# Performance work log

Hardware: AMD Instinct MI355X
Metric: run time of the kernel (lower is better)

Reference implementation:

```python
import jax, jax.numpy as jnp
import numpy as np

N_FFT = 2048
STRIDE = 512
FREQ_BINS = N_FFT  # __init__ passes freq_bins=n_fft


def _fourier_kernels():
    s = np.arange(N_FFT, dtype=np.float64)
    # scipy get_window('hann', n_fft, fftbins=True)
    win = 0.5 - 0.5 * np.cos(2.0 * np.pi * s / N_FFT)
    k = np.arange(FREQ_BINS, dtype=np.float64)
    phase = 2.0 * np.pi * np.outer(k, s) / N_FFT  # (bins, n_fft)
    wsin = (win * np.sin(phase)).astype(np.float32)
    wcos = (win * np.cos(phase)).astype(np.float32)
    return wsin, wcos


def setup_inputs() -> dict:
    key = jax.random.key(0)
    x = jax.random.normal(key, (8, 262144), dtype=jnp.float32)
    wsin, wcos = _fourier_kernels()
    return {"x": x, "wsin": jnp.asarray(wsin), "wcos": jnp.asarray(wcos)}


def reference(x, wsin, wcos):
    # center=True, pad_mode='reflect'
    xp = jnp.pad(x, ((0, 0), (N_FFT // 2, N_FFT // 2)), mode="reflect")
    num_frames = (xp.shape[1] - N_FFT) // STRIDE + 1
    # frame the signal: (batch, num_frames, n_fft)
    idx = np.arange(num_frames)[:, None] * STRIDE + np.arange(N_FFT)
    frames = xp[:, idx]
    # dense DFT as GEMM (equivalent to conv1d with sin/cos filters)
    imag = jnp.einsum("btn,kn->bkt", frames, wsin)
    real = jnp.einsum("btn,kn->bkt", frames, wcos)
    return (real, -imag)
```

## Files before the change

### kernel.cpp

```cpp
#include <hip/hip_runtime.h>
#include <hip/hip_bf16.h>
#include <stdint.h>

#define XLEN   262144
#define NT     513
#define NTP    528
#define NB     8
#define NCOL   (NB * NTP)
#define NKC4   320
#define KQ     512
#define NK     1088
#define NFFT   2048
#define OUTKT  (2048 * NT)
#define WSTR   ((size_t)NKC4 * KQ)
#define FSTR   ((size_t)NCOL * KQ)
#define PSTR   ((size_t)NKC4 * NCOL)

typedef __attribute__((ext_vector_type(8))) short short8;
typedef __attribute__((ext_vector_type(4))) short short4v;
typedef __attribute__((ext_vector_type(2))) short short2v;
typedef __attribute__((ext_vector_type(4))) float f32x4;

__device__ __forceinline__ short cvt_bf16(float f) {
  return __builtin_bit_cast(short, (__bf16)f);
}

__device__ __forceinline__ f32x4 bf4_to_f32(short4v v) {
  f32x4 o;
#pragma unroll
  for (int e = 0; e < 4; ++e) {
    uint32_t u = ((uint32_t)(uint16_t)v[e]) << 16;
    o[e] = __builtin_bit_cast(float, u);
  }
  return o;
}

__device__ __forceinline__ void gload16(const short* g, const short* l) {
  __builtin_amdgcn_global_load_lds(
      (const __attribute__((address_space(1))) void*)g,
      (__attribute__((address_space(3))) void*)l, 16, 0, 0);
}


__global__ __launch_bounds__(256) void conv_w_split4(
    const float* __restrict__ wsin, const float* __restrict__ wcos,
    short* __restrict__ wc4, short* __restrict__ ws4) {
  const int row = blockIdx.x;
  const int n0 = threadIdx.x * 8;
  const int m0 = n0 >> 2;
  short2v c[4], s[4];
  if (row <= 256) {
    const float* pc = wcos + (size_t)row * NFFT + n0;
    const float* ps = wsin + (size_t)row * NFFT + n0;
    f32x4 c0 = *(const f32x4*)pc, c1 = *(const f32x4*)(pc + 4);
    f32x4 s0 = *(const f32x4*)ps, s1 = *(const f32x4*)(ps + 4);
#pragma unroll
    for (int r = 0; r < 4; ++r) {
      c[r][0] = cvt_bf16(c0[r]); c[r][1] = cvt_bf16(c1[r]);
      s[r][0] = cvt_bf16(s0[r]); s[r][1] = cvt_bf16(s1[r]);
    }
  } else {
#pragma unroll
    for (int r = 0; r < 4; ++r) { c[r][0] = 0; c[r][1] = 0; s[r][0] = 0; s[r][1] = 0; }
  }
#pragma unroll
  for (int r = 0; r < 4; ++r) {
    *(short2v*)&wc4[r * WSTR + (size_t)row * KQ + m0] = c[r];
    *(short2v*)&ws4[r * WSTR + (size_t)row * KQ + m0] = s[r];
  }
}

__global__ __launch_bounds__(256) void conv_fr_split4(const float* __restrict__ x,
                                                      short* __restrict__ fr4) {
  const int j = blockIdx.x;
  const int b = j / NTP;
  const int t = j - b * NTP;
  const int n0 = threadIdx.x * 8;
  const int m0 = n0 >> 2;
  short2v v[4];
  if (t < NT) {
    const float* xb = x + (size_t)b * XLEN;
    const int q0 = t * 512 + n0 - 1024;
    float f[8];
    if (q0 >= 0 && q0 + 7 < XLEN) {
      *(f32x4*)(f)     = *(const f32x4*)(xb + q0);
      *(f32x4*)(f + 4) = *(const f32x4*)(xb + q0 + 4);
    } else {
#pragma unroll
      for (int e = 0; e < 8; ++e) {
        int mm = q0 + e;
        mm = (mm < 0) ? -mm : mm;
        mm = (mm >= XLEN) ? (2 * XLEN - 2 - mm) : mm;
        f[e] = xb[mm];
      }
    }
#pragma unroll
    for (int r = 0; r < 4; ++r) { v[r][0] = cvt_bf16(f[r]); v[r][1] = cvt_bf16(f[4 + r]); }
  } else {
#pragma unroll
    for (int r = 0; r < 4; ++r) { v[r][0] = 0; v[r][1] = 0; }
  }
#pragma unroll
  for (int r = 0; r < 4; ++r)
    *(short2v*)&fr4[r * FSTR + (size_t)j * KQ + m0] = v[r];
}

__global__ __launch_bounds__(256, 3) void dft_gemm_split4(
    const short* __restrict__ wc4, const short* __restrict__ ws4,
    const short* __restrict__ fr4,
    short* __restrict__ pC4, short* __restrict__ pS4) {
  __shared__ short lds[16384];

  const int tid  = threadIdx.x;
  const int lane = tid & 63;
  const int wid  = tid >> 6;

  const int o   = blockIdx.x;
  const int xcd = o & 7;
  const int i   = o >> 3;
  const int wg  = ((xcd < 4) ? xcd * 83 : 332 + (xcd - 4) * 82) + i;
  const int side = wg / 165;
  const int w    = wg - side * 165;
  const int k0   = (w % 5) * 64;
  const int j0   = (w / 5) * 128;

  const short* Ac = wc4 + side * WSTR;
  const short* As = ws4 + side * WSTR;
  const short* Bf = fr4 + side * FSTR;
  short* pC = pC4 + side * PSTR;
  short* pS = pS4 + side * PSTR;

  const int wrow = (wid >> 1) * 32;
  const int wcol = (wid & 1) * 64;

  f32x4 accC[2][4], accS[2][4];
#pragma unroll
  for (int m = 0; m < 2; ++m)
#pragma unroll
    for (int n = 0; n < 4; ++n) { accC[m][n] = (f32x4)0.0f; accS[m][n] = (f32x4)0.0f; }

  const int fr_r = lane & 15;
  const int srow = lane >> 3;
  const int scol = ((lane & 7) ^ srow) * 8;

  auto stage = [&](int n0) {
#pragma unroll
    for (int i2 = 0; i2 < 8; ++i2) {
      const int q = wid * 8 + i2;
      const short* src;
      int dst;
      if (q < 8) {
        src = Ac + (size_t)(k0 + q * 8 + srow) * KQ + n0 + scol;
        dst = q * 512;
      } else if (q < 16) {
        src = As + (size_t)(k0 + (q - 8) * 8 + srow) * KQ + n0 + scol;
        dst = 4096 + (q - 8) * 512;
      } else {
        src = Bf + (size_t)(j0 + (q - 16) * 8 + srow) * KQ + n0 + scol;
        dst = 8192 + (q - 16) * 512;
      }
      gload16(src, &lds[dst]);
    }
  };

  for (int ts = 0; ts < 8; ++ts) {
    if (ts) __syncthreads();
    stage(ts * 64);
    __syncthreads();
#pragma unroll
    for (int ks = 0; ks < 2; ++ks) {
      const int cc = ks * 4 + (lane >> 4);
      short8 aC[2], aS[2], bF[4];
#pragma unroll
      for (int m = 0; m < 2; ++m) {
        const int r = wrow + m * 16 + fr_r;
        const int off = (r << 6) + ((cc ^ (r & 7)) << 3);
        aC[m] = *(const short8*)&lds[off];
        aS[m] = *(const short8*)&lds[4096 + off];
      }
#pragma unroll
      for (int n = 0; n < 4; ++n) {
        const int r = wcol + n * 16 + fr_r;
        const int off = (r << 6) + ((cc ^ (r & 7)) << 3);
        bF[n] = *(const short8*)&lds[8192 + off];
      }
#pragma unroll
      for (int m = 0; m < 2; ++m)
#pragma unroll
        for (int n = 0; n < 4; ++n) {
          accC[m][n] = __builtin_amdgcn_mfma_f32_16x16x32_bf16(aC[m], bF[n], accC[m][n], 0, 0, 0);
          accS[m][n] = __builtin_amdgcn_mfma_f32_16x16x32_bf16(aS[m], bF[n], accS[m][n], 0, 0, 0);
        }
    }
  }

#pragma unroll
  for (int m = 0; m < 2; ++m) {
    const int row = k0 + wrow + m * 16 + (lane >> 4) * 4;
#pragma unroll
    for (int n = 0; n < 4; ++n) {
      const int col = j0 + wcol + n * 16 + (lane & 15);
      const size_t base = (size_t)row * NCOL + col;
#pragma unroll
      for (int r = 0; r < 4; ++r) {
        pC[base + (size_t)r * NCOL] = cvt_bf16(accC[m][n][r]);
        pS[base + (size_t)r * NCOL] = cvt_bf16(accS[m][n][r]);
      }
    }
  }
}

__global__ __launch_bounds__(256) void combine4_kernel(
    const short* __restrict__ pC4, const short* __restrict__ pS4,
    float* __restrict__ outR, float* __restrict__ outI) {
  const int k  = blockIdx.y;
  const int jq = blockIdx.x * 256 + threadIdx.x;
  if (jq >= NCOL / 4) return;
  const int j = jq * 4;
  const int b = j / NTP;
  const int t = j - b * NTP;
  const size_t pb = (size_t)k * NCOL + j;
  f32x4 C[4], S[4];
#pragma unroll
  for (int r = 0; r < 4; ++r) {
    C[r] = bf4_to_f32(*(const short4v*)&pC4[r * PSTR + pb]);
    S[r] = bf4_to_f32(*(const short4v*)&pS4[r * PSTR + pb]);
  }
  const f32x4 CA = C[0] + C[2], CB = C[1] + C[3];
  const f32x4 CmA = C[0] - C[2], CmB = C[1] - C[3];
  const f32x4 SA = S[0] + S[2], SB = S[1] + S[3];
  const f32x4 SmA = S[0] - S[2], SmB = S[1] - S[3];

  f32x4 Cw[4], Sw[4];
  Cw[0] = CA + CB;   Sw[0] = SA + SB;
  Cw[1] = CmA - SmB; Sw[1] = SmA + CmB;
  Cw[2] = CA - CB;   Sw[2] = SA - SB;
  Cw[3] = CmA + SmB; Sw[3] = SmA - CmB;

  const size_t ob = (size_t)b * OUTKT + t;
  const bool mir = (k >= 1) && (k <= 255);
#pragma unroll
  for (int jj = 0; jj < 4; ++jj) {
    const int rowD = 512 * jj + k;
    float* rD = outR + ob + (size_t)rowD * NT;
    float* iD = outI + ob + (size_t)rowD * NT;
    const int rowM = 512 * (4 - jj) - k;
    float* rM = outR + ob + (size_t)rowM * NT;
    float* iM = outI + ob + (size_t)rowM * NT;
#pragma unroll
    for (int e = 0; e < 4; ++e) {
      if (t + e < NT) {
        rD[e] = Cw[jj][e];
        iD[e] = -Sw[jj][e];
        if (mir) { rM[e] = Cw[jj][e]; iM[e] = Sw[jj][e]; }
      }
    }
  }
}


__global__ __launch_bounds__(256) void conv_w_kernel(const float* __restrict__ wsin,
                                                     const float* __restrict__ wcos,
                                                     short* __restrict__ wc,
                                                     short* __restrict__ ws) {
  const int row = blockIdx.x;
  const int c = threadIdx.x * 8;
  const float* src = (blockIdx.y ? wsin : wcos) + (size_t)row * NFFT + c;
  short* dst = (blockIdx.y ? ws : wc) + (size_t)row * NFFT + c;
  f32x4 a = *(const f32x4*)src;
  f32x4 b = *(const f32x4*)(src + 4);
  short8 o;
#pragma unroll
  for (int j = 0; j < 4; ++j) { o[j] = cvt_bf16(a[j]); o[4 + j] = cvt_bf16(b[j]); }
  *(short8*)dst = o;
}

__global__ __launch_bounds__(256) void conv_frames_kernel(const float* __restrict__ x,
                                                          short* __restrict__ fr) {
  const int j = blockIdx.x;
  const int b = j / NTP;
  const int t = j - b * NTP;
  const int c = threadIdx.x * 8;
  short8 o;
  if (t >= NT) {
#pragma unroll
    for (int k = 0; k < 8; ++k) o[k] = 0;
  } else {
    const float* xb = x + (size_t)b * XLEN;
    const int base = t * 512 + c - 1024;
    float v[8];
    if (base >= 0 && base + 7 < XLEN) {
      *(f32x4*)(v)     = *(const f32x4*)(xb + base);
      *(f32x4*)(v + 4) = *(const f32x4*)(xb + base + 4);
    } else {
#pragma unroll
      for (int k = 0; k < 8; ++k) {
        int m = base + k;
        m = (m < 0) ? -m : m;
        m = (m >= XLEN) ? (2 * XLEN - 2 - m) : m;
        v[k] = xb[m];
      }
    }
#pragma unroll
    for (int k = 0; k < 8; ++k) o[k] = cvt_bf16(v[k]);
  }
  *(short8*)&fr[(size_t)j * NFFT + c] = o;
}

__global__ __launch_bounds__(256, 3) void dft_gemm_r4(
    const short* __restrict__ wc_bf,
    const short* __restrict__ ws_bf,
    const short* __restrict__ fr_bf,
    float* __restrict__ outR,
    float* __restrict__ outI) {
  __shared__ short lds[16384];

  const int tid  = threadIdx.x;
  const int lane = tid & 63;
  const int wid  = tid >> 6;

  const int o   = blockIdx.x;
  const int xcd = o & 7;
  const int wg  = ((xcd < 1) ? xcd * 71 : 71 + (xcd - 1) * 70) + (o >> 3);
  const int k0  = (wg % 17) * 64;
  const int j0  = (wg / 17) * 128;

  const int wrow = (wid >> 1) * 32;
  const int wcol = (wid & 1) * 64;

  f32x4 accR[2][4], accI[2][4];
#pragma unroll
  for (int m = 0; m < 2; ++m)
#pragma unroll
    for (int n = 0; n < 4; ++n) { accR[m][n] = (f32x4)0.0f; accI[m][n] = (f32x4)0.0f; }

  const int fr_r = lane & 15;
  const int srow = lane >> 3;
  const int scol = ((lane & 7) ^ srow) * 8;

  auto stage = [&](int n0) {
#pragma unroll
    for (int i = 0; i < 8; ++i) {
      const int q = wid * 8 + i;
      const short* src;
      int dst;
      if (q < 8) {
        src = wc_bf + (size_t)(k0 + q * 8 + srow) * NFFT + n0 + scol;
        dst = q * 512;
      } else if (q < 16) {
        src = ws_bf + (size_t)(k0 + (q - 8) * 8 + srow) * NFFT + n0 + scol;
        dst = 4096 + (q - 8) * 512;
      } else {
        src = fr_bf + (size_t)(j0 + (q - 16) * 8 + srow) * NFFT + n0 + scol;
        dst = 8192 + (q - 16) * 512;
      }
      gload16(src, &lds[dst]);
    }
  };

  for (int t = 0; t < 32; ++t) {
    if (t) __syncthreads();
    stage(t * 64);
    __syncthreads();
#pragma unroll
    for (int ks = 0; ks < 2; ++ks) {
      const int cc = ks * 4 + (lane >> 4);
      short8 a_c[2], a_s[2], b_f[4];
#pragma unroll
      for (int m = 0; m < 2; ++m) {
        const int r = wrow + m * 16 + fr_r;
        const int off = (r << 6) + ((cc ^ (r & 7)) << 3);
        a_c[m] = *(const short8*)&lds[off];
        a_s[m] = *(const short8*)&lds[4096 + off];
      }
#pragma unroll
      for (int n = 0; n < 4; ++n) {
        const int r = wcol + n * 16 + fr_r;
        const int off = (r << 6) + ((cc ^ (r & 7)) << 3);
        b_f[n] = *(const short8*)&lds[8192 + off];
      }
#pragma unroll
      for (int m = 0; m < 2; ++m)
#pragma unroll
        for (int n = 0; n < 4; ++n) {
          accR[m][n] = __builtin_amdgcn_mfma_f32_16x16x32_bf16(a_c[m], b_f[n], accR[m][n], 0, 0, 0);
          accI[m][n] = __builtin_amdgcn_mfma_f32_16x16x32_bf16(a_s[m], b_f[n], accI[m][n], 0, 0, 0);
        }
    }
  }

#pragma unroll
  for (int m = 0; m < 2; ++m) {
    const int k = k0 + wrow + m * 16 + (lane >> 4) * 4;
#pragma unroll
    for (int n = 0; n < 4; ++n) {
      const int j = j0 + wcol + n * 16 + (lane & 15);
      const int b = j / NTP;
      const int t = j - b * NTP;
      if (t < NT) {
        const size_t base = (size_t)b * OUTKT + (size_t)k * NT + t;
#pragma unroll
        for (int r = 0; r < 4; ++r) {
          const int kk = k + r;
          const float vr = accR[m][n][r];
          const float vi = accI[m][n][r];
          outR[base + (size_t)r * NT] = vr;
          outI[base + (size_t)r * NT] = -vi;
          if (kk >= 1 && kk <= 960) {
            const size_t mb = (size_t)b * OUTKT + (size_t)(2048 - kk) * NT + t;
            outR[mb] = vr;
            outI[mb] = vi;
          }
        }
      }
    }
  }
}


extern "C" void kernel_launch(void* const* d_in, const int* in_sizes, int n_in,
                              void* d_out, int out_size, void* d_ws, size_t ws_size,
                              hipStream_t stream) {
  const float* x    = (const float*)d_in[0];
  const float* wsin = (const float*)d_in[1];
  const float* wcos = (const float*)d_in[2];
  float* outR = (float*)d_out;
  float* outI = outR + (size_t)NB * OUTKT;

  const size_t need4 = (8 * WSTR + 4 * FSTR + 8 * PSTR) * sizeof(short);

  if (ws_size >= need4) {
    short* wc4 = (short*)d_ws;
    short* ws4 = wc4 + 4 * WSTR;
    short* fr4 = ws4 + 4 * WSTR;
    short* pC4 = fr4 + 4 * FSTR;
    short* pS4 = pC4 + 4 * PSTR;

    conv_w_split4<<<NKC4, 256, 0, stream>>>(wsin, wcos, wc4, ws4);
    conv_fr_split4<<<NCOL, 256, 0, stream>>>(x, fr4);
    dft_gemm_split4<<<660, 256, 0, stream>>>(wc4, ws4, fr4, pC4, pS4);
    combine4_kernel<<<dim3(5, 257), 256, 0, stream>>>(pC4, pS4, outR, outI);
  } else {
    short* wc_bf = (short*)d_ws;
    short* ws_bf = wc_bf + (size_t)NK * NFFT;
    short* fr_bf = ws_bf + (size_t)NK * NFFT;
    conv_w_kernel<<<dim3(NK, 2), 256, 0, stream>>>(wsin, wcos, wc_bf, ws_bf);
    conv_frames_kernel<<<NCOL, 256, 0, stream>>>(x, fr_bf);
    dft_gemm_r4<<<561, 256, 0, stream>>>(wc_bf, ws_bf, fr_bf, outR, outI);
  }
}
```

Before: 61.66 us.

## Add radix-8 DFT decomposition path with split-8 GEMM and twiddle combine

Adds a radix-8 decimation path. The input frames and the first 129 DFT weight rows are split into 8 polyphase sub-sequences of length 256. Eight small GEMMs produce bf16 partials, and a combine kernel applies the 8-point twiddles and writes direct plus mirrored conjugate bins. This cuts GEMM FLOPs relative to the radix-4 path, in exchange for writing and reading more bf16 partial sums and doing more twiddle arithmetic in the combine step. The old radix-4 path becomes the fallback, and the full dense GEMM path is removed.

Result: slower. 64.02 us (+3.8%).

```diff
diff --git a/kernel.cpp b/kernel.cpp
--- a/kernel.cpp
+++ b/kernel.cpp
@@ -7,11 +7,17 @@
 #define NTP    528
 #define NB     8
 #define NCOL   (NB * NTP)
+#define NFFT   2048
+#define OUTKT  (2048 * NT)
+
+#define NKC8   192
+#define KO     256
+#define WSTR8  ((size_t)NKC8 * KO)
+#define FSTR8  ((size_t)NCOL * KO)
+#define PSTR8  ((size_t)NKC8 * NCOL)
+
 #define NKC4   320
 #define KQ     512
-#define NK     1088
-#define NFFT   2048
-#define OUTKT  (2048 * NT)
 #define WSTR   ((size_t)NKC4 * KQ)
 #define FSTR   ((size_t)NCOL * KQ)
 #define PSTR   ((size_t)NKC4 * NCOL)
@@ -39,6 +45,223 @@
   __builtin_amdgcn_global_load_lds(
       (const __attribute__((address_space(1))) void*)g,
       (__attribute__((address_space(3))) void*)l, 16, 0, 0);
+}
+
+
+__global__ __launch_bounds__(256) void conv_w_split8(
+    const float* __restrict__ wsin, const float* __restrict__ wcos,
+    short* __restrict__ wc8, short* __restrict__ ws8) {
+  const int row = blockIdx.x;
+  const int m = threadIdx.x;
+  const int n0 = m * 8;
+  short c[8], s[8];
+  if (row <= 128) {
+    const float* pc = wcos + (size_t)row * NFFT + n0;
+    const float* ps = wsin + (size_t)row * NFFT + n0;
+    f32x4 c0 = *(const f32x4*)pc, c1 = *(const f32x4*)(pc + 4);
+    f32x4 s0 = *(const f32x4*)ps, s1 = *(const f32x4*)(ps + 4);
+#pragma unroll
+    for (int r = 0; r < 4; ++r) {
+      c[r] = cvt_bf16(c0[r]); c[4 + r] = cvt_bf16(c1[r]);
+      s[r] = cvt_bf16(s0[r]); s[4 + r] = cvt_bf16(s1[r]);
+    }
+  } else {
+#pragma unroll
+    for (int r = 0; r < 8; ++r) { c[r] = 0; s[r] = 0; }
+  }
+  const size_t o = (size_t)row * KO + m;
+#pragma unroll
+  for (int r = 0; r < 8; ++r) {
+    wc8[r * WSTR8 + o] = c[r];
+    ws8[r * WSTR8 + o] = s[r];
+  }
+}
+
+__global__ __launch_bounds__(256) void conv_fr_split8(const float* __restrict__ x,
+                                                      short* __restrict__ fr8) {
+  const int j = blockIdx.x;
+  const int b = j / NTP;
+  const int t = j - b * NTP;
+  const int m = threadIdx.x;
+  short v[8];
+  if (t < NT) {
+    const float* xb = x + (size_t)b * XLEN;
+    const int q0 = t * 512 + m * 8 - 1024;
+    float f[8];
+    if (q0 >= 0 && q0 + 7 < XLEN) {
+      *(f32x4*)(f)     = *(const f32x4*)(xb + q0);
+      *(f32x4*)(f + 4) = *(const f32x4*)(xb + q0 + 4);
+    } else {
+#pragma unroll
+      for (int e = 0; e < 8; ++e) {
+        int mm = q0 + e;
+        mm = (mm < 0) ? -mm : mm;
+        mm = (mm >= XLEN) ? (2 * XLEN - 2 - mm) : mm;
+        f[e] = xb[mm];
+      }
+    }
+#pragma unroll
+    for (int r = 0; r < 8; ++r) v[r] = cvt_bf16(f[r]);
+  } else {
+#pragma unroll
+    for (int r = 0; r < 8; ++r) v[r] = 0;
+  }
+  const size_t o = (size_t)j * KO + m;
+#pragma unroll
+  for (int r = 0; r < 8; ++r) fr8[r * FSTR8 + o] = v[r];
+}
+
+__global__ __launch_bounds__(256, 4) void dft_gemm_split8(
+    const short* __restrict__ wc8, const short* __restrict__ ws8,
+    const short* __restrict__ fr8,
+    short* __restrict__ pC8, short* __restrict__ pS8) {
+  __shared__ short lds[16384];
+
+  const int tid  = threadIdx.x;
+  const int lane = tid & 63;
+  const int wid  = tid >> 6;
+
+  const int o   = blockIdx.x;
+  const int xcd = o & 7;
+  const int wg  = xcd * 99 + (o >> 3);
+  const int side = wg / 99;
+  const int w    = wg - side * 99;
+  const int k0   = (w % 3) * 64;
+  const int j0   = (w / 3) * 128;
+
+  const short* Ac = wc8 + side * WSTR8;
+  const short* As = ws8 + side * WSTR8;
+  const short* Bf = fr8 + side * FSTR8;
+  short* pC = pC8 + side * PSTR8;
+  short* pS = pS8 + side * PSTR8;
+
+  const int wrow = (wid >> 1) * 32;
+  const int wcol = (wid & 1) * 64;
+
+  f32x4 accC[2][4], accS[2][4];
+#pragma unroll
+  for (int m = 0; m < 2; ++m)
+#pragma unroll
+    for (int n = 0; n < 4; ++n) { accC[m][n] = (f32x4)0.0f; accS[m][n] = (f32x4)0.0f; }
+
+  const int fr_r = lane & 15;
+  const int srow = lane >> 3;
+  const int scol = ((lane & 7) ^ srow) * 8;
+
+  auto stage = [&](int n0) {
+#pragma unroll
+    for (int i2 = 0; i2 < 8; ++i2) {
+      const int q = wid * 8 + i2;
+      const short* src;
+      int dst;
+      if (q < 8) {
+        src = Ac + (size_t)(k0 + q * 8 + srow) * KO + n0 + scol;
+        dst = q * 512;
+      } else if (q < 16) {
+        src = As + (size_t)(k0 + (q - 8) * 8 + srow) * KO + n0 + scol;
+        dst = 4096 + (q - 8) * 512;
+      } else {
+        src = Bf + (size_t)(j0 + (q - 16) * 8 + srow) * KO + n0 + scol;
+        dst = 8192 + (q - 16) * 512;
+      }
+      gload16(src, &lds[dst]);
+    }
+  };
+
+  for (int ts = 0; ts < 4; ++ts) {
+    if (ts) __syncthreads();
+    stage(ts * 64);
+    __syncthreads();
+#pragma unroll
+    for (int ks = 0; ks < 2; ++ks) {
+      const int cc = ks * 4 + (lane >> 4);
+      short8 aC[2], aS[2], bF[4];
+#pragma unroll
+      for (int m = 0; m < 2; ++m) {
+        const int r = wrow + m * 16 + fr_r;
+        const int off = (r << 6) + ((cc ^ (r & 7)) << 3);
+        aC[m] = *(const short8*)&lds[off];
+        aS[m] = *(const short8*)&lds[4096 + off];
+      }
+#pragma unroll
+      for (int n = 0; n < 4; ++n) {
+        const int r = wcol + n * 16 + fr_r;
+        const int off = (r << 6) + ((cc ^ (r & 7)) << 3);
+        bF[n] = *(const short8*)&lds[8192 + off];
+      }
+#pragma unroll
+      for (int m = 0; m < 2; ++m)
+#pragma unroll
+        for (int n = 0; n < 4; ++n) {
+          accC[m][n] = __builtin_amdgcn_mfma_f32_16x16x32_bf16(aC[m], bF[n], accC[m][n], 0, 0, 0);
+          accS[m][n] = __builtin_amdgcn_mfma_f32_16x16x32_bf16(aS[m], bF[n], accS[m][n], 0, 0, 0);
+        }
+    }
+  }
+
+#pragma unroll
+  for (int m = 0; m < 2; ++m) {
+    const int row = k0 + wrow + m * 16 + (lane >> 4) * 4;
+#pragma unroll
+    for (int n = 0; n < 4; ++n) {
+      const int col = j0 + wcol + n * 16 + (lane & 15);
+      const size_t base = (size_t)row * NCOL + col;
+#pragma unroll
+      for (int r = 0; r < 4; ++r) {
+        pC[base + (size_t)r * NCOL] = cvt_bf16(accC[m][n][r]);
+        pS[base + (size_t)r * NCOL] = cvt_bf16(accS[m][n][r]);
+      }
+    }
+  }
+}
+
+__global__ __launch_bounds__(256) void combine8_kernel(
+    const short* __restrict__ pC8, const short* __restrict__ pS8,
+    float* __restrict__ outR, float* __restrict__ outI) {
+  const int k  = blockIdx.y;
+  const int jq = blockIdx.x * 256 + threadIdx.x;
+  if (jq >= NCOL / 4) return;
+  const int j = jq * 4;
+  const int b = j / NTP;
+  const int t = j - b * NTP;
+  const size_t pb = (size_t)k * NCOL + j;
+  f32x4 C[8], S[8];
+#pragma unroll
+  for (int r = 0; r < 8; ++r) {
+    C[r] = bf4_to_f32(*(const short4v*)&pC8[r * PSTR8 + pb]);
+    S[r] = bf4_to_f32(*(const short4v*)&pS8[r * PSTR8 + pb]);
+  }
+  const float RT2 = 0.70710678118654752f;
+  const float CT[8] = {1.f, RT2, 0.f, -RT2, -1.f, -RT2, 0.f, RT2};
+  const float ST[8] = {0.f, RT2, 1.f, RT2, 0.f, -RT2, -1.f, -RT2};
+
+  const size_t ob = (size_t)b * OUTKT + t;
+  const bool mir = (k >= 1) && (k <= 127);
+#pragma unroll
+  for (int jj = 0; jj < 8; ++jj) {
+    f32x4 Cw = (f32x4)0.0f, Sw = (f32x4)0.0f;
+#pragma unroll
+    for (int r = 0; r < 8; ++r) {
+      const float ct = CT[(jj * r) & 7];
+      const float st = ST[(jj * r) & 7];
+      Cw += ct * C[r] - st * S[r];
+      Sw += st * C[r] + ct * S[r];
+    }
+    const int rowD = 256 * jj + k;
+    float* rD = outR + ob + (size_t)rowD * NT;
+    float* iD = outI + ob + (size_t)rowD * NT;
+    const int rowM = 256 * (8 - jj) - k;
+    float* rM = outR + ob + (size_t)rowM * NT;
+    float* iM = outI + ob + (size_t)rowM * NT;
+#pragma unroll
+    for (int e = 0; e < 4; ++e) {
+      if (t + e < NT) {
+        rD[e] = Cw[e];
+        iD[e] = -Sw[e];
+        if (mir) { rM[e] = Cw[e]; iM[e] = Sw[e]; }
+      }
+    }
+  }
 }
 
 
@@ -63,10 +286,11 @@
 #pragma unroll
     for (int r = 0; r < 4; ++r) { c[r][0] = 0; c[r][1] = 0; s[r][0] = 0; s[r][1] = 0; }
   }
+  const size_t o = (size_t)row * KQ + m0;
 #pragma unroll
   for (int r = 0; r < 4; ++r) {
-    *(short2v*)&wc4[r * WSTR + (size_t)row * KQ + m0] = c[r];
-    *(short2v*)&ws4[r * WSTR + (size_t)row * KQ + m0] = s[r];
+    *(short2v*)&wc4[r * WSTR + o] = c[r];
+    *(short2v*)&ws4[r * WSTR + o] = s[r];
   }
 }
 
@@ -259,165 +483,6 @@
 }
 
 
-__global__ __launch_bounds__(256) void conv_w_kernel(const float* __restrict__ wsin,
-                                                     const float* __restrict__ wcos,
-                                                     short* __restrict__ wc,
-                                                     short* __restrict__ ws) {
-  const int row = blockIdx.x;
-  const int c = threadIdx.x * 8;
-  const float* src = (blockIdx.y ? wsin : wcos) + (size_t)row * NFFT + c;
-  short* dst = (blockIdx.y ? ws : wc) + (size_t)row * NFFT + c;
-  f32x4 a = *(const f32x4*)src;
-  f32x4 b = *(const f32x4*)(src + 4);
-  short8 o;
-#pragma unroll
-  for (int j = 0; j < 4; ++j) { o[j] = cvt_bf16(a[j]); o[4 + j] = cvt_bf16(b[j]); }
-  *(short8*)dst = o;
-}
-
-__global__ __launch_bounds__(256) void conv_frames_kernel(const float* __restrict__ x,
-                                                          short* __restrict__ fr) {
-  const int j = blockIdx.x;
-  const int b = j / NTP;
-  const int t = j - b * NTP;
-  const int c = threadIdx.x * 8;
-  short8 o;
-  if (t >= NT) {
-#pragma unroll
-    for (int k = 0; k < 8; ++k) o[k] = 0;
-  } else {
-    const float* xb = x + (size_t)b * XLEN;
-    const int base = t * 512 + c - 1024;
-    float v[8];
-    if (base >= 0 && base + 7 < XLEN) {
-      *(f32x4*)(v)     = *(const f32x4*)(xb + base);
-      *(f32x4*)(v + 4) = *(const f32x4*)(xb + base + 4);
-    } else {
-#pragma unroll
-      for (int k = 0; k < 8; ++k) {
-        int m = base + k;
-        m = (m < 0) ? -m : m;
-        m = (m >= XLEN) ? (2 * XLEN - 2 - m) : m;
-        v[k] = xb[m];
-      }
-    }
-#pragma unroll
-    for (int k = 0; k < 8; ++k) o[k] = cvt_bf16(v[k]);
-  }
-  *(short8*)&fr[(size_t)j * NFFT + c] = o;
-}
-
-__global__ __launch_bounds__(256, 3) void dft_gemm_r4(
-    const short* __restrict__ wc_bf,
-    const short* __restrict__ ws_bf,
-    const short* __restrict__ fr_bf,
-    float* __restrict__ outR,
-    float* __restrict__ outI) {
-  __shared__ short lds[16384];
-
-  const int tid  = threadIdx.x;
-  const int lane = tid & 63;
-  const int wid  = tid >> 6;
-
-  const int o   = blockIdx.x;
-  const int xcd = o & 7;
-  const int wg  = ((xcd < 1) ? xcd * 71 : 71 + (xcd - 1) * 70) + (o >> 3);
-  const int k0  = (wg % 17) * 64;
-  const int j0  = (wg / 17) * 128;
-
-  const int wrow = (wid >> 1) * 32;
-  const int wcol = (wid & 1) * 64;
-
-  f32x4 accR[2][4], accI[2][4];
-#pragma unroll
-  for (int m = 0; m < 2; ++m)
-#pragma unroll
-    for (int n = 0; n < 4; ++n) { accR[m][n] = (f32x4)0.0f; accI[m][n] = (f32x4)0.0f; }
-
-  const int fr_r = lane & 15;
-  const int srow = lane >> 3;
-  const int scol = ((lane & 7) ^ srow) * 8;
-
-  auto stage = [&](int n0) {
-#pragma unroll
-    for (int i = 0; i < 8; ++i) {
-      const int q = wid * 8 + i;
-      const short* src;
-      int dst;
-      if (q < 8) {
-        src = wc_bf + (size_t)(k0 + q * 8 + srow) * NFFT + n0 + scol;
-        dst = q * 512;
-      } else if (q < 16) {
-        src = ws_bf + (size_t)(k0 + (q - 8) * 8 + srow) * NFFT + n0 + scol;
-        dst = 4096 + (q - 8) * 512;
-      } else {
-        src = fr_bf + (size_t)(j0 + (q - 16) * 8 + srow) * NFFT + n0 + scol;
-        dst = 8192 + (q - 16) * 512;
-      }
-      gload16(src, &lds[dst]);
-    }
-  };
-
-  for (int t = 0; t < 32; ++t) {
-    if (t) __syncthreads();
-    stage(t * 64);
-    __syncthreads();
-#pragma unroll
-    for (int ks = 0; ks < 2; ++ks) {
-      const int cc = ks * 4 + (lane >> 4);
-      short8 a_c[2], a_s[2], b_f[4];
-#pragma unroll
-      for (int m = 0; m < 2; ++m) {
-        const int r = wrow + m * 16 + fr_r;
-        const int off = (r << 6) + ((cc ^ (r & 7)) << 3);
-        a_c[m] = *(const short8*)&lds[off];
-        a_s[m] = *(const short8*)&lds[4096 + off];
-      }
-#pragma unroll
-      for (int n = 0; n < 4; ++n) {
-        const int r = wcol + n * 16 + fr_r;
-        const int off = (r << 6) + ((cc ^ (r & 7)) << 3);
-        b_f[n] = *(const short8*)&lds[8192 + off];
-      }
-#pragma unroll
-      for (int m = 0; m < 2; ++m)
-#pragma unroll
-        for (int n = 0; n < 4; ++n) {
-          accR[m][n] = __builtin_amdgcn_mfma_f32_16x16x32_bf16(a_c[m], b_f[n], accR[m][n], 0, 0, 0);
-          accI[m][n] = __builtin_amdgcn_mfma_f32_16x16x32_bf16(a_s[m], b_f[n], accI[m][n], 0, 0, 0);
-        }
-    }
-  }
-
-#pragma unroll
-  for (int m = 0; m < 2; ++m) {
-    const int k = k0 + wrow + m * 16 + (lane >> 4) * 4;
-#pragma unroll
-    for (int n = 0; n < 4; ++n) {
-      const int j = j0 + wcol + n * 16 + (lane & 15);
-      const int b = j / NTP;
-      const int t = j - b * NTP;
-      if (t < NT) {
-        const size_t base = (size_t)b * OUTKT + (size_t)k * NT + t;
-#pragma unroll
-        for (int r = 0; r < 4; ++r) {
-          const int kk = k + r;
-          const float vr = accR[m][n][r];
-          const float vi = accI[m][n][r];
-          outR[base + (size_t)r * NT] = vr;
-          outI[base + (size_t)r * NT] = -vi;
-          if (kk >= 1 && kk <= 960) {
-            const size_t mb = (size_t)b * OUTKT + (size_t)(2048 - kk) * NT + t;
-            outR[mb] = vr;
-            outI[mb] = vi;
-          }
-        }
-      }
-    }
-  }
-}
-
-
 extern "C" void kernel_launch(void* const* d_in, const int* in_sizes, int n_in,
                               void* d_out, int out_size, void* d_ws, size_t ws_size,
                               hipStream_t stream) {
@@ -427,9 +492,20 @@
   float* outR = (float*)d_out;
   float* outI = outR + (size_t)NB * OUTKT;
 
-  const size_t need4 = (8 * WSTR + 4 * FSTR + 8 * PSTR) * sizeof(short);
-
-  if (ws_size >= need4) {
+  const size_t need8 = (16 * WSTR8 + 8 * FSTR8 + 16 * PSTR8) * sizeof(short);
+
+  if (ws_size >= need8) {
+    short* wc8 = (short*)d_ws;
+    short* ws8 = wc8 + 8 * WSTR8;
+    short* fr8 = ws8 + 8 * WSTR8;
+    short* pC8 = fr8 + 8 * FSTR8;
+    short* pS8 = pC8 + 8 * PSTR8;
+
+    conv_w_split8<<<NKC8, 256, 0, stream>>>(wsin, wcos, wc8, ws8);
+    conv_fr_split8<<<NCOL, 256, 0, stream>>>(x, fr8);
+    dft_gemm_split8<<<792, 256, 0, stream>>>(wc8, ws8, fr8, pC8, pS8);
+    combine8_kernel<<<dim3(5, 129), 256, 0, stream>>>(pC8, pS8, outR, outI);
+  } else {
     short* wc4 = (short*)d_ws;
     short* ws4 = wc4 + 4 * WSTR;
     short* fr4 = ws4 + 4 * WSTR;
@@ -440,12 +516,5 @@
     conv_fr_split4<<<NCOL, 256, 0, stream>>>(x, fr4);
     dft_gemm_split4<<<660, 256, 0, stream>>>(wc4, ws4, fr4, pC4, pS4);
     combine4_kernel<<<dim3(5, 257), 256, 0, stream>>>(pC4, pS4, outR, outI);
-  } else {
-    short* wc_bf = (short*)d_ws;
-    short* ws_bf = wc_bf + (size_t)NK * NFFT;
-    short* fr_bf = ws_bf + (size_t)NK * NFFT;
-    conv_w_kernel<<<dim3(NK, 2), 256, 0, stream>>>(wsin, wcos, wc_bf, ws_bf);
-    conv_frames_kernel<<<NCOL, 256, 0, stream>>>(x, fr_bf);
-    dft_gemm_r4<<<561, 256, 0, stream>>>(wc_bf, ws_bf, fr_bf, outR, outI);
-  }
-}
+  }
+}
```
